# Performance work log

Measured on AMD Instinct MI355X. Metric: run time of the kernel, lower is better.

Reference implementation:

```python
import jax, jax.numpy as jnp
import numpy as np

EPS = 1e-5

def _bn(x, gamma, beta):
    # training-mode BatchNorm1d over (batch, points) per channel; x: [B, C, N]
    mean = x.mean(axis=(0, 2), keepdims=True)
    var = x.var(axis=(0, 2), keepdims=True)
    return gamma[None, :, None] * (x - mean) * jax.lax.rsqrt(var + EPS) + beta[None, :, None]

def _conv_nn(x, idx, W, b):
    # x: [B, Cin, N_in]; idx: [N_out, k]; W: [Cout, Cin, k]
    g = x[:, :, idx]  # gather -> [B, Cin, N_out, k]
    return jnp.einsum('bink,oik->bon', g, W) + b[None, :, None]

def setup_inputs() -> dict:
    key = jax.random.key(0)
    ks = jax.random.split(key, 8)
    B, Cin, Cout = 32, 32, 64
    Nin, Nout, K, KP = 32768, 8192, 9, 4
    s = 0.05
    return {
        'x': jax.random.normal(ks[0], (B, Cin, Nin), jnp.float32),
        'W1': jax.random.normal(ks[1], (Cout, Cin, K), jnp.float32) * s,
        'b1': jnp.zeros((Cout,), jnp.float32),
        'W2': jax.random.normal(ks[2], (Cout, Cout, K), jnp.float32) * s,
        'b2': jnp.zeros((Cout,), jnp.float32),
        'We': jax.random.normal(ks[3], (Cout, Cin), jnp.float32) * s,
        'be': jnp.zeros((Cout,), jnp.float32),
        'g1': jnp.ones((Cout,), jnp.float32), 'beta1': jnp.zeros((Cout,), jnp.float32),
        'g2': jnp.ones((Cout,), jnp.float32), 'beta2': jnp.zeros((Cout,), jnp.float32),
        'g3': jnp.ones((Cout,), jnp.float32), 'beta3': jnp.zeros((Cout,), jnp.float32),
        'idx1': jax.random.randint(ks[4], (Nout, K), 0, Nin, jnp.int32),
        'idx2': jax.random.randint(ks[5], (Nout, K), 0, Nout, jnp.int32),
        'pool_idx': jax.random.randint(ks[6], (Nout, KP), 0, Nin, jnp.int32),
    }

def reference(x, W1, b1, W2, b2, We, be, g1, beta1, g2, beta2, g3, beta3, idx1, idx2, pool_idx):
    # main branch: ConvNN -> BN -> ReLU -> ConvNN -> BN
    out = jax.nn.relu(_bn(_conv_nn(x, idx1, W1, b1), g1, beta1))
    out = _bn(_conv_nn(out, idx2, W2, b2), g2, beta2)
    # shortcut: AvgPoolNN (k=4) -> 1x1 conv expand -> BN
    pooled = x[:, :, pool_idx].mean(axis=-1)  # [B, Cin, N_out]
    identity = _bn(jnp.einsum('bin,oi->bon', pooled, We) + be[None, :, None], g3, beta3)
    return jax.nn.relu(out + identity)
```

## Files before the change

### kernel.cpp

```cpp
#include <hip/hip_runtime.h>
#include <hip/hip_bf16.h>

typedef __attribute__((ext_vector_type(8))) short short8_t;
typedef __attribute__((ext_vector_type(4))) float f32x4_t;

#define NOUT 8192
#define NIN 32768
#define MTOT 262144.0f
#define ST_STRIPES 64

#define MF(a,b,c) __builtin_amdgcn_mfma_f32_16x16x32_bf16((a),(b),(c),0,0,0)

static __device__ __forceinline__ float bf2f(ushort u) {
    union { float f; unsigned int i; } x; x.i = ((unsigned int)u) << 16; return x.f;
}
static __device__ __forceinline__ ushort f2bfx(float f) {
    union { __hip_bfloat16 h; ushort u; } v;
    v.h = __float2bfloat16(f);
    return v.u;
}
static __device__ __forceinline__ short8_t i4s8(int4 v) {
    union { int4 i; short8_t s; } u; u.i = v; return u.s;
}

static __device__ __forceinline__ short8_t bn8(int4 v, const float* a8, const float* c8) {
    ushort* pv = (ushort*)&v;
    #pragma unroll
    for (int e = 0; e < 8; ++e)
        pv[e] = f2bfx(fmaxf(a8[e] * bf2f(pv[e]) + c8[e], 0.f));
    return i4s8(v);
}

__global__ __launch_bounds__(256) void transpose_x_kernel(
    const float* __restrict__ x, ushort* __restrict__ xt)
{
    __shared__ ushort T[64][66];
    const int tid = threadIdx.x;
    const int n0 = blockIdx.x * 64, c0 = blockIdx.y * 64;
    const int lane64 = tid & 63, rb = (tid >> 6) * 16;
    #pragma unroll
    for (int r = 0; r < 16; ++r) {
        int c_l = rb + r;
        T[c_l][lane64] = f2bfx(x[(size_t)(c0 + c_l) * NIN + n0 + lane64]);
    }
    __syncthreads();
    #pragma unroll
    for (int r = 0; r < 16; ++r) {
        int n_l = rb + r;
        xt[(size_t)(n0 + n_l) * 1024 + c0 + lane64] = T[lane64][n_l];
    }
}

__global__ __launch_bounds__(256) void prep_w_kernel(
    const float* __restrict__ W1, const float* __restrict__ W2,
    const float* __restrict__ We,
    ushort* __restrict__ w1p, ushort* __restrict__ w2p, ushort* __restrict__ wep,
    float* __restrict__ stz)
{
    int t = blockIdx.x * 256 + threadIdx.x;
    const int N1 = 18432, N2 = 36864, N3 = 2048;
    if (t < 3 * ST_STRIPES * 128) stz[t] = 0.f;
    if (t < N1) {
        int e = t & 7, o = (t >> 3) & 63, seg = t >> 9;
        int fcg = seg & 3, k = seg >> 2;
        int i = fcg * 8 + e;
        w1p[t] = f2bfx(W1[o * 288 + i * 9 + k]);
    } else if (t < N1 + N2) {
        int t2 = t - N1;
        int e = t2 & 7, o = (t2 >> 3) & 63, seg = t2 >> 9;
        int fcg = seg & 3, kk = (seg >> 2) & 1, k = seg >> 3;
        int ci = kk * 32 + fcg * 8 + e;
        w2p[t2] = f2bfx(W2[o * 576 + ci * 9 + k]);
    } else if (t < N1 + N2 + N3) {
        int t3 = t - N1 - N2;
        wep[t3] = f2bfx(We[t3]);
    }
}

__global__ __launch_bounds__(512, 2) void conv1i_kernel(
    const ushort* __restrict__ xt, const int* __restrict__ idx1,
    const int* __restrict__ pool_idx, const ushort* __restrict__ w1p,
    const ushort* __restrict__ wep,
    ushort* __restrict__ out1, ushort* __restrict__ identt,
    float* __restrict__ st1g, float* __restrict__ st3g)
{
    __shared__ __align__(16) ushort Wl[18432];
    __shared__ float Ls1[128], Ls3[128];
    const int tid = threadIdx.x;
    const int lane = tid & 63, wv = tid >> 6;
    const int n = __builtin_amdgcn_readfirstlane(blockIdx.x * 8 + wv);
    const int l15 = lane & 15, fcg = lane >> 4, fc = fcg * 8;

    for (int i = tid; i < 2304; i += 512)
        ((int4*)Wl)[i] = ((const int4*)w1p)[i];
    if (tid < 128) { Ls1[tid] = 0.f; Ls3[tid] = 0.f; }

    int rows[9], prow[4];
    {
        const int* idxn = idx1 + n * 9;
        #pragma unroll
        for (int t = 0; t < 9; ++t) rows[t] = idxn[t];
        const int* pn = pool_idx + n * 4;
        #pragma unroll
        for (int t = 0; t < 4; ++t) prow[t] = pn[t];
    }
    __syncthreads();

    f32x4_t acc[2][4];
    #pragma unroll
    for (int m = 0; m < 2; ++m)
        #pragma unroll
        for (int nt = 0; nt < 4; ++nt) acc[m][nt] = (f32x4_t){0.f, 0.f, 0.f, 0.f};

    int4 A0[2], A1[2], A2[2], A3[2];

#define C1_PRE(K, A) { \
    const ushort* rp = xt + (size_t)rows[K] * 1024 + l15 * 32 + fc; \
    A[0] = *(const int4*)rp; \
    A[1] = *(const int4*)(rp + 512); }

#define C1_PPRE(KP, A) { \
    const ushort* rp = xt + (size_t)prow[KP] * 1024 + l15 * 32 + fc; \
    A[0] = *(const int4*)rp; \
    A[1] = *(const int4*)(rp + 512); }

#define C1_BODY(K, A) { \
    const ushort* wp = Wl + ((K) * 4 + fcg) * 512; \
    short8_t b0 = *(const short8_t*)(wp + l15 * 8); \
    short8_t b1 = *(const short8_t*)(wp + (16 + l15) * 8); \
    short8_t b2 = *(const short8_t*)(wp + (32 + l15) * 8); \
    short8_t b3 = *(const short8_t*)(wp + (48 + l15) * 8); \
    short8_t af0 = i4s8(A[0]), af1 = i4s8(A[1]); \
    acc[0][0] = MF(af0, b0, acc[0][0]); acc[1][0] = MF(af1, b0, acc[1][0]); \
    acc[0][1] = MF(af0, b1, acc[0][1]); acc[1][1] = MF(af1, b1, acc[1][1]); \
    acc[0][2] = MF(af0, b2, acc[0][2]); acc[1][2] = MF(af1, b2, acc[1][2]); \
    acc[0][3] = MF(af0, b3, acc[0][3]); acc[1][3] = MF(af1, b3, acc[1][3]); }

    C1_PRE(0, A0); C1_PRE(1, A1); C1_PRE(2, A2); C1_PRE(3, A3);
    C1_BODY(0, A0); C1_PRE(4, A0);
    C1_BODY(1, A1); C1_PRE(5, A1);
    C1_BODY(2, A2); C1_PRE(6, A2);
    C1_BODY(3, A3); C1_PRE(7, A3);
    C1_BODY(4, A0); C1_PRE(8, A0);
    C1_BODY(5, A1); C1_PPRE(0, A1);
    C1_BODY(6, A2); C1_PPRE(1, A2);
    C1_BODY(7, A3); C1_PPRE(2, A3);
    C1_BODY(8, A0);
#undef C1_PRE
#undef C1_BODY

    const size_t outbase = (size_t)n * 2048;
    #pragma unroll
    for (int m = 0; m < 2; ++m)
        #pragma unroll
        for (int nt = 0; nt < 4; ++nt)
            #pragma unroll
            for (int j = 0; j < 4; ++j) {
                int b = m * 16 + (lane >> 4) * 4 + j;
                int o = nt * 16 + l15;
                out1[outbase + b * 64 + o] = f2bfx(acc[m][nt][j]);
            }
    #pragma unroll
    for (int nt = 0; nt < 4; ++nt) {
        float s = 0.f, q = 0.f;
        #pragma unroll
        for (int m = 0; m < 2; ++m)
            #pragma unroll
            for (int j = 0; j < 4; ++j) { float v = acc[m][nt][j]; s += v; q += v * v; }
        s += __shfl_xor(s, 16); s += __shfl_xor(s, 32);
        q += __shfl_xor(q, 16); q += __shfl_xor(q, 32);
        if (lane < 16) {
            atomicAdd(&Ls1[nt * 16 + lane], s);
            atomicAdd(&Ls1[64 + nt * 16 + lane], q);
        }
    }

    int4 P3[2];
    C1_PPRE(3, P3);
#undef C1_PPRE
    float s0[8], s1[8];
    #pragma unroll
    for (int e = 0; e < 8; ++e) { s0[e] = 0.f; s1[e] = 0.f; }
    {
        const ushort* p;
        p = (const ushort*)&A1[0];
        #pragma unroll
        for (int e = 0; e < 8; ++e) s0[e] += bf2f(p[e]);
        p = (const ushort*)&A1[1];
        #pragma unroll
        for (int e = 0; e < 8; ++e) s1[e] += bf2f(p[e]);
        p = (const ushort*)&A2[0];
        #pragma unroll
        for (int e = 0; e < 8; ++e) s0[e] += bf2f(p[e]);
        p = (const ushort*)&A2[1];
        #pragma unroll
        for (int e = 0; e < 8; ++e) s1[e] += bf2f(p[e]);
        p = (const ushort*)&A3[0];
        #pragma unroll
        for (int e = 0; e < 8; ++e) s0[e] += bf2f(p[e]);
        p = (const ushort*)&A3[1];
        #pragma unroll
        for (int e = 0; e < 8; ++e) s1[e] += bf2f(p[e]);
        p = (const ushort*)&P3[0];
        #pragma unroll
        for (int e = 0; e < 8; ++e) s0[e] += bf2f(p[e]);
        p = (const ushort*)&P3[1];
        #pragma unroll
        for (int e = 0; e < 8; ++e) s1[e] += bf2f(p[e]);
    }
    short8_t paf0, paf1;
    {
        int4 v0, v1; ushort* p0 = (ushort*)&v0; ushort* p1 = (ushort*)&v1;
        #pragma unroll
        for (int e = 0; e < 8; ++e) {
            p0[e] = f2bfx(s0[e] * 0.25f);
            p1[e] = f2bfx(s1[e] * 0.25f);
        }
        paf0 = i4s8(v0); paf1 = i4s8(v1);
    }
    short8_t bfr[4];
    {
        const ushort* wpf = wep + l15 * 32 + fc;
        #pragma unroll
        for (int nt = 0; nt < 4; ++nt)
            bfr[nt] = *(const short8_t*)(wpf + nt * 512);
    }
    #pragma unroll
    for (int nt = 0; nt < 4; ++nt) {
        acc[0][nt] = (f32x4_t){0.f, 0.f, 0.f, 0.f};
        acc[1][nt] = (f32x4_t){0.f, 0.f, 0.f, 0.f};
        acc[0][nt] = MF(paf0, bfr[nt], acc[0][nt]);
        acc[1][nt] = MF(paf1, bfr[nt], acc[1][nt]);
    }
    #pragma unroll
    for (int m = 0; m < 2; ++m)
        #pragma unroll
        for (int nt = 0; nt < 4; ++nt)
            #pragma unroll
            for (int j = 0; j < 4; ++j) {
                int b = m * 16 + (lane >> 4) * 4 + j;
                int o = nt * 16 + l15;
                identt[outbase + b * 64 + o] = f2bfx(acc[m][nt][j]);
            }
    #pragma unroll
    for (int nt = 0; nt < 4; ++nt) {
        float s = 0.f, q = 0.f;
        #pragma unroll
        for (int m = 0; m < 2; ++m)
            #pragma unroll
            for (int j = 0; j < 4; ++j) { float v = acc[m][nt][j]; s += v; q += v * v; }
        s += __shfl_xor(s, 16); s += __shfl_xor(s, 32);
        q += __shfl_xor(q, 16); q += __shfl_xor(q, 32);
        if (lane < 16) {
            atomicAdd(&Ls3[nt * 16 + lane], s);
            atomicAdd(&Ls3[64 + nt * 16 + lane], q);
        }
    }
    __syncthreads();
    if (tid < 128) {
        atomicAdd(&st1g[(blockIdx.x & (ST_STRIPES - 1)) * 128 + tid], Ls1[tid]);
        atomicAdd(&st3g[(blockIdx.x & (ST_STRIPES - 1)) * 128 + tid], Ls3[tid]);
    }
}

__global__ __launch_bounds__(512, 2) void conv2_kernel(
    const ushort* __restrict__ out1raw, const int* __restrict__ idx2,
    const ushort* __restrict__ w2p, const float* __restrict__ ac1,
    ushort* __restrict__ out2, float* __restrict__ st)
{
    __shared__ __align__(16) ushort Wl[36864];
    __shared__ float Ls[128];
    const int tid = threadIdx.x;
    const int lane = tid & 63, wv = tid >> 6;
    const int n = __builtin_amdgcn_readfirstlane(blockIdx.x * 8 + wv);
    const int l15 = lane & 15, fcg = lane >> 4, fc = fcg * 8;

    for (int i = tid; i < 4608; i += 512)
        ((int4*)Wl)[i] = ((const int4*)w2p)[i];
    if (tid < 128) Ls[tid] = 0.f;

    int rows[9];
    {
        const int* idxn = idx2 + n * 9;
        #pragma unroll
        for (int t = 0; t < 9; ++t) rows[t] = idxn[t];
    }
    float a0r[8], c0r[8], a1r[8], c1r[8];
    #pragma unroll
    for (int e = 0; e < 8; ++e) {
        a0r[e] = ac1[fc + e];       c0r[e] = ac1[64 + fc + e];
        a1r[e] = ac1[32 + fc + e];  c1r[e] = ac1[96 + fc + e];
    }
    __syncthreads();

    f32x4_t acc[2][4];
    #pragma unroll
    for (int m = 0; m < 2; ++m)
        #pragma unroll
        for (int nt = 0; nt < 4; ++nt) acc[m][nt] = (f32x4_t){0.f, 0.f, 0.f, 0.f};

    int4 A0[4], A1[4], A2[4];

#define C2_PRE(K, A) { \
    const ushort* rp = out1raw + (size_t)rows[K] * 2048 + l15 * 64 + fc; \
    A[0] = *(const int4*)rp; \
    A[1] = *(const int4*)(rp + 32); \
    A[2] = *(const int4*)(rp + 1024); \
    A[3] = *(const int4*)(rp + 1056); }

#define C2_BODY(K, A) { \
    const ushort* wp0 = Wl + ((K) * 8 + fcg) * 512; \
    const ushort* wp1 = wp0 + 2048; \
    short8_t b00 = *(const short8_t*)(wp0 + l15 * 8); \
    short8_t b10 = *(const short8_t*)(wp0 + (16 + l15) * 8); \
    short8_t b20 = *(const short8_t*)(wp0 + (32 + l15) * 8); \
    short8_t b30 = *(const short8_t*)(wp0 + (48 + l15) * 8); \
    short8_t b01 = *(const short8_t*)(wp1 + l15 * 8); \
    short8_t b11 = *(const short8_t*)(wp1 + (16 + l15) * 8); \
    short8_t b21 = *(const short8_t*)(wp1 + (32 + l15) * 8); \
    short8_t b31 = *(const short8_t*)(wp1 + (48 + l15) * 8); \
    short8_t af00 = bn8(A[0], a0r, c0r); \
    short8_t af01 = bn8(A[1], a1r, c1r); \
    short8_t af10 = bn8(A[2], a0r, c0r); \
    short8_t af11 = bn8(A[3], a1r, c1r); \
    acc[0][0] = MF(af00, b00, acc[0][0]); acc[0][0] = MF(af01, b01, acc[0][0]); \
    acc[0][1] = MF(af00, b10, acc[0][1]); acc[0][1] = MF(af01, b11, acc[0][1]); \
    acc[0][2] = MF(af00, b20, acc[0][2]); acc[0][2] = MF(af01, b21, acc[0][2]); \
    acc[0][3] = MF(af00, b30, acc[0][3]); acc[0][3] = MF(af01, b31, acc[0][3]); \
    acc[1][0] = MF(af10, b00, acc[1][0]); acc[1][0] = MF(af11, b01, acc[1][0]); \
    acc[1][1] = MF(af10, b10, acc[1][1]); acc[1][1] = MF(af11, b11, acc[1][1]); \
    acc[1][2] = MF(af10, b20, acc[1][2]); acc[1][2] = MF(af11, b21, acc[1][2]); \
    acc[1][3] = MF(af10, b30, acc[1][3]); acc[1][3] = MF(af11, b31, acc[1][3]); }

    C2_PRE(0, A0); C2_PRE(1, A1); C2_PRE(2, A2);
    C2_BODY(0, A0); C2_PRE(3, A0);
    C2_BODY(1, A1); C2_PRE(4, A1);
    C2_BODY(2, A2); C2_PRE(5, A2);
    C2_BODY(3, A0); C2_PRE(6, A0);
    C2_BODY(4, A1); C2_PRE(7, A1);
    C2_BODY(5, A2); C2_PRE(8, A2);
    C2_BODY(6, A0);
    C2_BODY(7, A1);
    C2_BODY(8, A2);
#undef C2_PRE
#undef C2_BODY

    const size_t outbase = (size_t)n * 2048;
    #pragma unroll
    for (int m = 0; m < 2; ++m)
        #pragma unroll
        for (int nt = 0; nt < 4; ++nt)
            #pragma unroll
            for (int j = 0; j < 4; ++j) {
                int b = m * 16 + (lane >> 4) * 4 + j;
                int o = nt * 16 + l15;
                out2[outbase + b * 64 + o] = f2bfx(acc[m][nt][j]);
            }
    #pragma unroll
    for (int nt = 0; nt < 4; ++nt) {
        float s = 0.f, q = 0.f;
        #pragma unroll
        for (int m = 0; m < 2; ++m)
            #pragma unroll
            for (int j = 0; j < 4; ++j) { float v = acc[m][nt][j]; s += v; q += v * v; }
        s += __shfl_xor(s, 16); s += __shfl_xor(s, 32);
        q += __shfl_xor(q, 16); q += __shfl_xor(q, 32);
        if (lane < 16) {
            atomicAdd(&Ls[nt * 16 + lane], s);
            atomicAdd(&Ls[64 + nt * 16 + lane], q);
        }
    }
    __syncthreads();
    if (tid < 128) atomicAdd(&st[(blockIdx.x & (ST_STRIPES - 1)) * 128 + tid], Ls[tid]);
}

__global__ void finalize_kernel(const float* __restrict__ st, const float* __restrict__ g,
                                const float* __restrict__ bet, float* __restrict__ ac)
{
    int o = threadIdx.x;
    if (o >= 64) return;
    float s = 0.f, q = 0.f;
    for (int i = 0; i < ST_STRIPES; ++i) { s += st[i * 128 + o]; q += st[i * 128 + 64 + o]; }
    float mean = s * (1.0f / MTOT);
    float var  = q * (1.0f / MTOT) - mean * mean;
    float a = g[o] * rsqrtf(var + 1e-5f);
    ac[o] = a;
    ac[64 + o] = bet[o] - a * mean;
}

__global__ void finalize_dual_kernel(
    const float* __restrict__ stA, const float* __restrict__ gA, const float* __restrict__ bA,
    const float* __restrict__ stB, const float* __restrict__ gB, const float* __restrict__ bB,
    float* __restrict__ acA, float* __restrict__ acB)
{
    int o = threadIdx.x;
    if (o >= 64) return;
    const float* st = blockIdx.x ? stB : stA;
    const float* g  = blockIdx.x ? gB  : gA;
    const float* bt = blockIdx.x ? bB  : bA;
    float* ac       = blockIdx.x ? acB : acA;
    float s = 0.f, q = 0.f;
    for (int i = 0; i < ST_STRIPES; ++i) { s += st[i * 128 + o]; q += st[i * 128 + 64 + o]; }
    float mean = s * (1.0f / MTOT);
    float var  = q * (1.0f / MTOT) - mean * mean;
    float a = g[o] * rsqrtf(var + 1e-5f);
    ac[o] = a;
    ac[64 + o] = bt[o] - a * mean;
}

__global__ __launch_bounds__(256) void final_combine_kernel(
    const ushort* __restrict__ out2, const ushort* __restrict__ idt,
    const float* __restrict__ ac2, const float* __restrict__ ac3,
    float* __restrict__ dout)
{
    __shared__ float tile[64][65];
    const int tid = threadIdx.x;
    const int n0 = blockIdx.x * 64, bo0 = blockIdx.y * 64;
    const int lane64 = tid & 63, rb = (tid >> 6) * 16;
    const int o = lane64;
    const float a2 = ac2[o], c2 = ac2[64 + o], a3 = ac3[o], c3 = ac3[64 + o];
    #pragma unroll
    for (int r = 0; r < 16; ++r) {
        int n_l = rb + r;
        size_t p = (size_t)(n0 + n_l) * 2048 + bo0 + lane64;
        float v = a2 * bf2f(out2[p]) + c2 + a3 * bf2f(idt[p]) + c3;
        tile[n_l][lane64] = fmaxf(v, 0.f);
    }
    __syncthreads();
    #pragma unroll
    for (int r = 0; r < 16; ++r) {
        int bo_l = rb + r;
        dout[(size_t)(bo0 + bo_l) * NOUT + n0 + lane64] = tile[lane64][bo_l];
    }
}

extern "C" void kernel_launch(void* const* d_in, const int* in_sizes, int n_in,
                              void* d_out, int out_size, void* d_ws, size_t ws_size,
                              hipStream_t stream)
{
    const float* x     = (const float*)d_in[0];
    const float* W1    = (const float*)d_in[1];
    const float* W2    = (const float*)d_in[3];
    const float* We    = (const float*)d_in[5];
    const float* g1    = (const float*)d_in[7];
    const float* beta1 = (const float*)d_in[8];
    const float* g2    = (const float*)d_in[9];
    const float* beta2 = (const float*)d_in[10];
    const float* g3    = (const float*)d_in[11];
    const float* beta3 = (const float*)d_in[12];
    const int* idx1    = (const int*)d_in[13];
    const int* idx2    = (const int*)d_in[14];
    const int* pool_idx= (const int*)d_in[15];
    float* dout = (float*)d_out;

    char* ws = (char*)d_ws;
    const size_t off_xt   = 0;
    const size_t off_out1 = 67108864;
    const size_t off_out2 = 100663296;
    const size_t off_id   = 134217728;
    const size_t off_w1p  = 167772160;
    const size_t off_w2p  = 167809024;
    const size_t off_wep  = 167882752;
    const size_t off_st   = 167886848;
    const size_t off_ac   = 167985152;
    const size_t need     = 167986688;
    if (ws_size < need) return;

    ushort* xt   = (ushort*)(ws + off_xt);
    ushort* out1 = (ushort*)(ws + off_out1);
    ushort* out2 = (ushort*)(ws + off_out2);
    ushort* idt  = (ushort*)(ws + off_id);
    ushort* w1p  = (ushort*)(ws + off_w1p);
    ushort* w2p  = (ushort*)(ws + off_w2p);
    ushort* wep  = (ushort*)(ws + off_wep);
    float*  st1  = (float*)(ws + off_st);
    float*  st2  = st1 + 64 * 128;
    float*  st3  = st1 + 2 * 64 * 128;
    float*  ac1  = (float*)(ws + off_ac);
    float*  ac2  = ac1 + 128;
    float*  ac3  = ac1 + 256;

    prep_w_kernel<<<224, 256, 0, stream>>>(W1, W2, We, w1p, w2p, wep, st1);
    transpose_x_kernel<<<dim3(512, 16), 256, 0, stream>>>(x, xt);
    conv1i_kernel<<<1024, 512, 0, stream>>>(xt, idx1, pool_idx, w1p, wep, out1, idt, st1, st3);
    finalize_dual_kernel<<<2, 64, 0, stream>>>(st1, g1, beta1, st3, g3, beta3, ac1, ac3);
    conv2_kernel<<<1024, 512, 0, stream>>>(out1, idx2, w2p, ac1, out2, st2);
    finalize_kernel<<<1, 64, 0, stream>>>(st2, g2, beta2, ac2);
    final_combine_kernel<<<dim3(128, 32), 256, 0, stream>>>(out2, idt, ac2, ac3, dout);
}
```

Baseline: 172.7 us.

## Slice conv1 output by batch groups so conv2 gathers stay cache-local

Conv1 now writes its output in a layout split into eight slices of four batches each, so each slice is a compact array of points. Conv2 blocks each handle one batch slice across 64 points, so the MFMA M dimension spans 8 points times 4 batches instead of 32 batches of one point. Because each gathered row is now 512 bytes inside a 4 MB slice, the random idx2 gathers for a block touch a much smaller working set, which should improve L2 hit rates. The cost is that each lane loads its own neighbor indices and there are more scattered 64-byte reads, and the output store pattern in conv2 changes.

```diff
diff --git a/kernel.cpp b/kernel.cpp
--- a/kernel.cpp
+++ b/kernel.cpp
@@ -8,6 +8,7 @@
 #define NIN 32768
 #define MTOT 262144.0f
 #define ST_STRIPES 64
+#define SLICE 2097152
 
 #define MF(a,b,c) __builtin_amdgcn_mfma_f32_16x16x32_bf16((a),(b),(c),0,0,0)
 
@@ -149,7 +150,6 @@
 #undef C1_PRE
 #undef C1_BODY
 
-    const size_t outbase = (size_t)n * 2048;
     #pragma unroll
     for (int m = 0; m < 2; ++m)
         #pragma unroll
@@ -158,7 +158,8 @@
             for (int j = 0; j < 4; ++j) {
                 int b = m * 16 + (lane >> 4) * 4 + j;
                 int o = nt * 16 + l15;
-                out1[outbase + b * 64 + o] = f2bfx(acc[m][nt][j]);
+                out1[(size_t)(b >> 2) * SLICE + (size_t)n * 256 + (b & 3) * 64 + o]
+                    = f2bfx(acc[m][nt][j]);
             }
     #pragma unroll
     for (int nt = 0; nt < 4; ++nt) {
@@ -232,6 +233,7 @@
         acc[0][nt] = MF(paf0, bfr[nt], acc[0][nt]);
         acc[1][nt] = MF(paf1, bfr[nt], acc[1][nt]);
     }
+    const size_t outbase = (size_t)n * 2048;
     #pragma unroll
     for (int m = 0; m < 2; ++m)
         #pragma unroll
@@ -272,18 +274,22 @@
     __shared__ float Ls[128];
     const int tid = threadIdx.x;
     const int lane = tid & 63, wv = tid >> 6;
-    const int n = __builtin_amdgcn_readfirstlane(blockIdx.x * 8 + wv);
+    const int bh = __builtin_amdgcn_readfirstlane(blockIdx.x & 7);
+    const int n0 = __builtin_amdgcn_readfirstlane((blockIdx.x >> 3) * 64 + wv * 8);
     const int l15 = lane & 15, fcg = lane >> 4, fc = fcg * 8;
+    const int bl = l15 & 3;
+    const ushort* out1s = out1raw + (size_t)bh * SLICE;
 
     for (int i = tid; i < 4608; i += 512)
         ((int4*)Wl)[i] = ((const int4*)w2p)[i];
     if (tid < 128) Ls[tid] = 0.f;
 
-    int rows[9];
+    int r0[9], r1[9];
     {
-        const int* idxn = idx2 + n * 9;
-        #pragma unroll
-        for (int t = 0; t < 9; ++t) rows[t] = idxn[t];
+        const int* ip0 = idx2 + (n0 + (l15 >> 2)) * 9;
+        const int* ip1 = ip0 + 36;
+        #pragma unroll
+        for (int t = 0; t < 9; ++t) { r0[t] = ip0[t]; r1[t] = ip1[t]; }
     }
     float a0r[8], c0r[8], a1r[8], c1r[8];
     #pragma unroll
@@ -302,11 +308,12 @@
     int4 A0[4], A1[4], A2[4];
 
 #define C2_PRE(K, A) { \
-    const ushort* rp = out1raw + (size_t)rows[K] * 2048 + l15 * 64 + fc; \
-    A[0] = *(const int4*)rp; \
-    A[1] = *(const int4*)(rp + 32); \
-    A[2] = *(const int4*)(rp + 1024); \
-    A[3] = *(const int4*)(rp + 1056); }
+    const ushort* rp0 = out1s + (size_t)r0[K] * 256 + bl * 64 + fc; \
+    const ushort* rp1 = out1s + (size_t)r1[K] * 256 + bl * 64 + fc; \
+    A[0] = *(const int4*)rp0; \
+    A[1] = *(const int4*)(rp0 + 32); \
+    A[2] = *(const int4*)rp1; \
+    A[3] = *(const int4*)(rp1 + 32); }
 
 #define C2_BODY(K, A) { \
     const ushort* wp0 = Wl + ((K) * 8 + fcg) * 512; \
@@ -345,16 +352,16 @@
 #undef C2_PRE
 #undef C2_BODY
 
-    const size_t outbase = (size_t)n * 2048;
     #pragma unroll
     for (int m = 0; m < 2; ++m)
         #pragma unroll
         for (int nt = 0; nt < 4; ++nt)
             #pragma unroll
             for (int j = 0; j < 4; ++j) {
-                int b = m * 16 + (lane >> 4) * 4 + j;
+                int nn = n0 + m * 4 + (lane >> 4);
+                int bcol = bh * 4 + j;
                 int o = nt * 16 + l15;
-                out2[outbase + b * 64 + o] = f2bfx(acc[m][nt][j]);
+                out2[(size_t)nn * 2048 + bcol * 64 + o] = f2bfx(acc[m][nt][j]);
             }
     #pragma unroll
     for (int nt = 0; nt < 4; ++nt) {
```

After: 183.8 us. +6.4%, slower.
